# Performance work log

Hardware: AMD Instinct MI355X
Metric: run time of the kernel (lower is better)

## Reference

```python
import jax, jax.numpy as jnp
import numpy as np

N, E, DIN, DH, DOUT, NB = 50000, 400000, 32, 128, 16, 2

def setup_inputs() -> dict:
    key = jax.random.key(0)
    ks = jax.random.split(key, 16)
    s = 0.05
    inp = {
        "inputs": jax.random.normal(ks[0], (N, DIN), jnp.float32),
        "frames": jax.random.normal(ks[1], (N, 3, 3), jnp.float32),
        "edge_index": jax.random.randint(ks[2], (2, E), 0, N, jnp.int32),
        # GraphNet in/out projections
        "win": jax.random.normal(ks[3], (DIN, DH), jnp.float32) * s,
        "bin_": jnp.zeros((DH,), jnp.float32),
        "wout": jax.random.normal(ks[4], (DH, DOUT), jnp.float32) * s,
        "bout": jnp.zeros((DOUT,), jnp.float32),
        # per-block EdgeConv params, stacked over NB blocks
        # mlp1: Linear(2*DH, DH) -> ReLU -> Linear(DH, DH) -> ReLU -> Linear(DH, DH)
        "w1a": jax.random.normal(ks[5], (NB, 2 * DH, DH), jnp.float32) * s,
        "b1a": jnp.zeros((NB, DH), jnp.float32),
        "w1b": jax.random.normal(ks[6], (NB, DH, DH), jnp.float32) * s,
        "b1b": jnp.zeros((NB, DH), jnp.float32),
        "w1c": jax.random.normal(ks[7], (NB, DH, DH), jnp.float32) * s,
        "b1c": jnp.zeros((NB, DH), jnp.float32),
        # mlp2: Linear(DH, DH) -> ReLU -> Linear(DH, DH)
        "w2a": jax.random.normal(ks[8], (NB, DH, DH), jnp.float32) * s,
        "b2a": jnp.zeros((NB, DH), jnp.float32),
        "w2b": jax.random.normal(ks[9], (NB, DH, DH), jnp.float32) * s,
        "b2b": jnp.zeros((NB, DH), jnp.float32),
    }
    return inp


def reference(inputs, frames, edge_index, win, bin_, wout, bout,
              w1a, b1a, w1b, b1b, w1c, b1c, w2a, b2a, w2b, b2b):
    src = edge_index[0]  # j: message source
    dst = edge_index[1]  # i: aggregation target (PyG convention)
    x = inputs @ win + bin_  # [N, DH]
    for b in range(NB):
        x_j = x[src]  # [E, DH] gather
        x_i = x[dst]  # [E, DH] gather
        m = jnp.concatenate([x_j, x_i], axis=-1)  # [E, 2*DH]
        m = jax.nn.relu(m @ w1a[b] + b1a[b])
        m = jax.nn.relu(m @ w1b[b] + b1b[b])
        m = m @ w1c[b] + b1c[b]  # [E, DH]
        agg = jax.ops.segment_sum(m, dst, num_segments=N)  # aggr='add'
        h = jax.nn.relu(agg @ w2a[b] + b2a[b])
        x = h @ w2b[b] + b2b[b]
    return x @ wout + bout  # [N, DOUT]
```

## Files before the change

### kernel.cpp

```cpp
#include <hip/hip_runtime.h>

#define NN 50000
#define NE 400000
#define DIN 32
#define DH  128
#define DOUT 16
#define NB  2
#define NBLK 49

typedef _Float16 half8 __attribute__((ext_vector_type(8)));
typedef float    f32x4 __attribute__((ext_vector_type(4)));

#define FENCE() asm volatile("s_waitcnt lgkmcnt(0)" ::: "memory")
#define MFMA16(a, b, c) __builtin_amdgcn_mfma_f32_16x16x32_f16((a), (b), (c), 0, 0, 0)

__global__ void k_node_proj(const float* __restrict__ inp,
                            const float* __restrict__ win,
                            const float* __restrict__ bin,
                            _Float16* __restrict__ x16) {
    int gid = blockIdx.x * blockDim.x + threadIdx.x;
    if (gid >= NN * DH) return;
    int n = gid >> 7, h = gid & 127;
    float acc = bin[h];
    const float* row = inp + (size_t)n * DIN;
#pragma unroll
    for (int k = 0; k < DIN; ++k) acc = fmaf(row[k], win[k * DH + h], acc);
    x16[gid] = (_Float16)acc;
}

__global__ void k_wprep(const float* __restrict__ w1a, const float* __restrict__ w1b,
                        const float* __restrict__ w1c, const float* __restrict__ w2a,
                        const float* __restrict__ w2b, _Float16* __restrict__ wf) {
    int c = blockIdx.x * blockDim.x + threadIdx.x;
    if (c >= NB * 12288) return;
    int b = c / 12288, r = c % 12288;
    int tt = r >> 9, rem = r & 511;
    const float* W; int t;
    if (tt < 8)       { W = w1a + (size_t)b * 2 * DH * DH; t = tt; }
    else if (tt < 12) { W = w1b + (size_t)b * DH * DH; t = tt - 8; }
    else if (tt < 16) { W = w1c + (size_t)b * DH * DH; t = tt - 12; }
    else if (tt < 20) { W = w2a + (size_t)b * DH * DH; t = tt - 16; }
    else              { W = w2b + (size_t)b * DH * DH; t = tt - 20; }
    bool perm = (tt >= 8 && tt < 16);
    int n = rem >> 6, l = rem & 63;
    int col = n * 16 + (l & 15);
    half8 v;
#pragma unroll
    for (int j = 0; j < 8; ++j) {
        int row = perm ? ((2 * t + (j >> 2)) * 16 + (l >> 4) * 4 + (j & 3))
                       : (t * 32 + (l >> 4) * 8 + j);
        v[j] = (_Float16)W[(size_t)row * DH + col];
    }
    *(half8*)(wf + (size_t)c * 8) = v;
}

__global__ void k_woutprep(const float* __restrict__ wout, _Float16* __restrict__ wf) {
    int c = threadIdx.x;
    int t = c >> 6, l = c & 63;
    half8 v;
#pragma unroll
    for (int j = 0; j < 8; ++j)
        v[j] = (_Float16)wout[(size_t)(t * 32 + (l >> 4) * 8 + j) * DOUT + (l & 15)];
    *(half8*)(wf + (size_t)c * 8) = v;
}

__global__ void k_hist(const int* __restrict__ dstI, int* __restrict__ deg) {
    int e = blockIdx.x * blockDim.x + threadIdx.x;
    if (e < NE) atomicAdd(&deg[dstI[e]], 1);
}

__global__ void __launch_bounds__(1024) k_scanA(const int* __restrict__ deg,
                                                int* __restrict__ bsum) {
    __shared__ int ws[16];
    int tid = threadIdx.x, wv = tid >> 6, l = tid & 63;
    int i = blockIdx.x * 1024 + tid;
    int v = (i < NN) ? deg[i] : 0;
#pragma unroll
    for (int off = 32; off; off >>= 1) v += __shfl_down(v, off);
    if (l == 0) ws[wv] = v;
    __syncthreads();
    if (tid == 0) {
        int s = 0;
#pragma unroll
        for (int k = 0; k < 16; ++k) s += ws[k];
        bsum[blockIdx.x] = s;
    }
}

__global__ void k_scanB(const int* __restrict__ bsum, int* __restrict__ boff) {
    int l = threadIdx.x;
    int v = (l < NBLK) ? bsum[l] : 0;
    int s = v;
#pragma unroll
    for (int off = 1; off < 64; off <<= 1) {
        int t = __shfl_up(s, off);
        if (l >= off) s += t;
    }
    if (l < NBLK) boff[l] = s - v;
}

__global__ void __launch_bounds__(1024) k_scanC(const int* __restrict__ deg,
                                                const int* __restrict__ boff,
                                                int* __restrict__ cur) {
    __shared__ int ws[16];
    int tid = threadIdx.x, wv = tid >> 6, l = tid & 63;
    int i = blockIdx.x * 1024 + tid;
    int v = (i < NN) ? deg[i] : 0;
    int s = v;
#pragma unroll
    for (int off = 1; off < 64; off <<= 1) {
        int t = __shfl_up(s, off);
        if (l >= off) s += t;
    }
    if (l == 63) ws[wv] = s;
    __syncthreads();
    if (wv == 0) {
        int t = (l < 16) ? ws[l] : 0;
#pragma unroll
        for (int off = 1; off < 16; off <<= 1) {
            int u = __shfl_up(t, off);
            if (l >= off) t += u;
        }
        if (l < 16) ws[l] = t;
    }
    __syncthreads();
    int base = boff[blockIdx.x] + (wv ? ws[wv - 1] : 0);
    if (i < NN) cur[i] = base + s - v;
}

__global__ void k_scatter(const int* __restrict__ srcI, const int* __restrict__ dstI,
                          int* __restrict__ cur, int* __restrict__ eS,
                          int* __restrict__ eD) {
    int e = blockIdx.x * blockDim.x + threadIdx.x;
    if (e >= NE) return;
    int d = dstI[e];
    int p = atomicAdd(&cur[d], 1);
    eS[p] = srcI[e];
    eD[p] = d;
}

__global__ void __launch_bounds__(256, 4) k_edge8(
    const _Float16* __restrict__ xin,
    const int* __restrict__ eS, const int* __restrict__ eD,
    const half8* __restrict__ wfa, const half8* __restrict__ wfb,
    const half8* __restrict__ wfc,
    const float* __restrict__ b1a, const float* __restrict__ b1b,
    const float* __restrict__ b1c,
    float* __restrict__ agg) {
    __shared__ _Float16 sm[8192];
    __shared__ int slotT[4][64];

    const int tid = threadIdx.x, wv = tid >> 6, l = tid & 63;
    const int lm = l & 15, lk = l >> 4;
    const int nb = wv * 2;
    const int ebase = blockIdx.x * 64;

    int srcs[4], dsts[4];
#pragma unroll
    for (int s = 0; s < 4; ++s) {
        srcs[s] = eS[ebase + s * 16 + lm];
        dsts[s] = eD[ebase + s * 16 + lm];
    }

    int dl = eD[ebase + l];
    int prev = __shfl(dl, (l == 0) ? 0 : l - 1);
    bool bit = ((l & 31) == 0) ? true : (dl != prev);
    unsigned long long bal = __ballot(bit);
    unsigned mlo = (unsigned)bal, mhi = (unsigned)(bal >> 32);
    unsigned myM = (l < 32) ? mlo : mhi;
    int ll = l & 31;
    int slot_l = __popc(myM << (31 - ll)) - 1;
    if (bit) slotT[wv][(l >> 5) * 32 + slot_l] = dl;
    int nlo = __popc(mlo), nhi = __popc(mhi);

    const f32x4 z = {0.f, 0.f, 0.f, 0.f};
    f32x4 acc[4][2];
    half8 aC[4], aN[4], wC[2], wN[2];

#pragma unroll
    for (int s = 0; s < 4; ++s)
#pragma unroll
        for (int q = 0; q < 2; ++q) acc[s][q] = z;
#pragma unroll
    for (int s = 0; s < 4; ++s)
        aC[s] = *(const half8*)(xin + (size_t)srcs[s] * DH + lk * 8);
#pragma unroll
    for (int q = 0; q < 2; ++q) wC[q] = wfa[(size_t)(nb + q) * 64 + l];

    for (int t = 0; t < 8; ++t) {
        if (t < 7) {
            int t1 = t + 1;
#pragma unroll
            for (int s = 0; s < 4; ++s) {
                int node = (t1 < 4) ? srcs[s] : dsts[s];
                aN[s] = *(const half8*)(xin + (size_t)node * DH + (t1 & 3) * 32 + lk * 8);
            }
#pragma unroll
            for (int q = 0; q < 2; ++q)
                wN[q] = wfa[(size_t)(t1 * 8 + nb + q) * 64 + l];
        }
#pragma unroll
        for (int q = 0; q < 2; ++q)
#pragma unroll
            for (int s = 0; s < 4; ++s)
                acc[s][q] = MFMA16(wC[q], aC[s], acc[s][q]);
#pragma unroll
        for (int s = 0; s < 4; ++s) aC[s] = aN[s];
#pragma unroll
        for (int q = 0; q < 2; ++q) wC[q] = wN[q];
    }
    {
        float4 B0 = *(const float4*)(b1a + nb * 16 + lk * 4);
        float4 B1 = *(const float4*)(b1a + (nb + 1) * 16 + lk * 4);
#pragma unroll
        for (int s = 0; s < 4; ++s) {
            half8 v;
#pragma unroll
            for (int j = 0; j < 4; ++j) {
                v[j]     = (_Float16)fmaxf(acc[s][0][j] + (&B0.x)[j], 0.f);
                v[4 + j] = (_Float16)fmaxf(acc[s][1][j] + (&B1.x)[j], 0.f);
            }
            *(half8*)&sm[((wv * 4 + s) * 64 + l) * 8] = v;
        }
    }
    __syncthreads();

#pragma unroll
    for (int s = 0; s < 4; ++s)
#pragma unroll
        for (int q = 0; q < 2; ++q) acc[s][q] = z;
#pragma unroll
    for (int q = 0; q < 2; ++q) wC[q] = wfb[(size_t)(nb + q) * 64 + l];
    for (int t = 0; t < 4; ++t) {
        if (t < 3)
#pragma unroll
            for (int q = 0; q < 2; ++q)
                wN[q] = wfb[(size_t)((t + 1) * 8 + nb + q) * 64 + l];
#pragma unroll
        for (int s = 0; s < 4; ++s)
            aC[s] = *(const half8*)&sm[((t * 4 + s) * 64 + l) * 8];
#pragma unroll
        for (int q = 0; q < 2; ++q)
#pragma unroll
            for (int s = 0; s < 4; ++s)
                acc[s][q] = MFMA16(wC[q], aC[s], acc[s][q]);
#pragma unroll
        for (int q = 0; q < 2; ++q) wC[q] = wN[q];
    }
    __syncthreads();
    {
        float4 B0 = *(const float4*)(b1b + nb * 16 + lk * 4);
        float4 B1 = *(const float4*)(b1b + (nb + 1) * 16 + lk * 4);
#pragma unroll
        for (int s = 0; s < 4; ++s) {
            half8 v;
#pragma unroll
            for (int j = 0; j < 4; ++j) {
                v[j]     = (_Float16)fmaxf(acc[s][0][j] + (&B0.x)[j], 0.f);
                v[4 + j] = (_Float16)fmaxf(acc[s][1][j] + (&B1.x)[j], 0.f);
            }
            *(half8*)&sm[((wv * 4 + s) * 64 + l) * 8] = v;
        }
    }
    __syncthreads();

#pragma unroll
    for (int s = 0; s < 4; ++s)
#pragma unroll
        for (int q = 0; q < 2; ++q) acc[s][q] = z;
#pragma unroll
    for (int q = 0; q < 2; ++q) wC[q] = wfc[(size_t)(nb + q) * 64 + l];
    for (int t = 0; t < 4; ++t) {
        if (t < 3)
#pragma unroll
            for (int q = 0; q < 2; ++q)
                wN[q] = wfc[(size_t)((t + 1) * 8 + nb + q) * 64 + l];
#pragma unroll
        for (int s = 0; s < 4; ++s)
            aC[s] = *(const half8*)&sm[((t * 4 + s) * 64 + l) * 8];
#pragma unroll
        for (int q = 0; q < 2; ++q)
#pragma unroll
            for (int s = 0; s < 4; ++s)
                acc[s][q] = MFMA16(wC[q], aC[s], acc[s][q]);
#pragma unroll
        for (int q = 0; q < 2; ++q) wC[q] = wN[q];
    }
    __syncthreads();

    {
        float4 C0 = *(const float4*)(b1c + nb * 16 + lk * 4);
        float4 C1 = *(const float4*)(b1c + (nb + 1) * 16 + lk * 4);
#pragma unroll
        for (int s = 0; s < 4; ++s) {
            int h = s >> 1;
            int ldb = (s & 1) * 32 + (lm >> 3) * 16;
#pragma unroll
            for (int q = 0; q < 2; ++q) {
#pragma unroll
                for (int j = 0; j < 4; ++j) {
                    int idx = wv * 2048 +
                              ((h * 2 + q) * 64 + ldb + lk * 4 + j) * 8 + (lm & 7);
                    idx ^= (lm >> 3) << 4;
                    float bv = q ? (&C1.x)[j] : (&C0.x)[j];
                    sm[idx] = (_Float16)(acc[s][q][j] + bv);
                }
            }
        }
    }
    FENCE();

#pragma unroll
    for (int h = 0; h < 2; ++h) {
        const int nsl = h ? nhi : nlo;
        half8 ind0, ind1;
#pragma unroll
        for (int e8 = 0; e8 < 8; ++e8) {
            int se = __shfl(slot_l, h * 32 + lk * 8 + e8);
            ind0[e8] = (se == lm)      ? (_Float16)1.f : (_Float16)0.f;
            ind1[e8] = (se == lm + 16) ? (_Float16)1.f : (_Float16)0.f;
        }
        int4 dv  = *(const int4*)&slotT[wv][h * 32 + lk * 4];
        int4 dv2 = *(const int4*)&slotT[wv][h * 32 + 16 + lk * 4];
        int dS[4], dS2[4];
#pragma unroll
        for (int r = 0; r < 4; ++r) {
            int s0 = lk * 4 + r;
            dS[r]  = (s0 < nsl && s0 < 16) ? (&dv.x)[r] : -1;
            dS2[r] = (16 + s0 < nsl) ? (&dv2.x)[r] : -1;
        }
#pragma unroll
        for (int q = 0; q < 2; ++q) {
            int g = nb + q;
            int bidx = (wv * 2048 + ((h * 2 + q) * 64 + l) * 8) ^ (((l >> 4) & 1) << 4);
            half8 bfrag = *(const half8*)&sm[bidx];
            f32x4 p = MFMA16(ind0, bfrag, z);
#pragma unroll
            for (int r = 0; r < 4; ++r)
                if (dS[r] >= 0)
                    unsafeAtomicAdd(agg + (size_t)dS[r] * DH + g * 16 + lm, p[r]);
            if (nsl > 16) {
                f32x4 p2 = MFMA16(ind1, bfrag, z);
#pragma unroll
                for (int r = 0; r < 4; ++r)
                    if (dS2[r] >= 0)
                        unsafeAtomicAdd(agg + (size_t)dS2[r] * DH + g * 16 + lm, p2[r]);
            }
        }
    }
}

template <bool LAST>
__global__ void __launch_bounds__(256, 4) k_node_mfma(
    const float* __restrict__ agg,
    const half8* __restrict__ wfa, const half8* __restrict__ wfb,
    const float* __restrict__ b2a, const float* __restrict__ b2b,
    _Float16* __restrict__ xo,
    const half8* __restrict__ woutf, const float* __restrict__ bout,
    float* __restrict__ out) {
    __shared__ _Float16 sM[4][2048];
    const int tid = threadIdx.x, wv = tid >> 6, l = tid & 63;
    const int lm = l & 15, lk = l >> 4;
    const int n0 = (blockIdx.x * 4 + wv) * 16;
    if (n0 >= NN) return;
    int nodeA = n0 + lm;
    if (nodeA >= NN) nodeA = NN - 1;

    float b2ar[8], b2br[8];
#pragma unroll
    for (int n = 0; n < 8; ++n) {
        b2ar[n] = b2a[n * 16 + lm];
        b2br[n] = b2b[n * 16 + lm];
    }

    const f32x4 z = {0.f, 0.f, 0.f, 0.f};
    f32x4 acc[8];
#pragma unroll
    for (int n = 0; n < 8; ++n) acc[n] = z;

    for (int t = 0; t < 4; ++t) {
        const float* ap = agg + (size_t)nodeA * DH + t * 32 + lk * 8;
        float4 v0 = *(const float4*)ap;
        float4 v1 = *(const float4*)(ap + 4);
        half8 a;
        a[0] = (_Float16)v0.x; a[1] = (_Float16)v0.y;
        a[2] = (_Float16)v0.z; a[3] = (_Float16)v0.w;
        a[4] = (_Float16)v1.x; a[5] = (_Float16)v1.y;
        a[6] = (_Float16)v1.z; a[7] = (_Float16)v1.w;
        const half8* wp = wfa + (size_t)t * 512 + l;
#pragma unroll
        for (int n = 0; n < 8; ++n) acc[n] = MFMA16(a, wp[n * 64], acc[n]);
    }
    _Float16* sm = sM[wv];
#pragma unroll
    for (int n = 0; n < 8; ++n) {
        int base = ((n >> 1) * 64 + ((n & 1) * 2 + (lm >> 3)) * 16 + lk * 4) * 8 +
                   (lm & 7);
#pragma unroll
        for (int j = 0; j < 4; ++j)
            sm[base + j * 8] = (_Float16)fmaxf(acc[n][j] + b2ar[n], 0.f);
    }
    FENCE();
#pragma unroll
    for (int n = 0; n < 8; ++n) acc[n] = z;
    for (int t = 0; t < 4; ++t) {
        half8 a = *(const half8*)&sm[(t * 64 + l) * 8];
        const half8* wp = wfb + (size_t)t * 512 + l;
#pragma unroll
        for (int n = 0; n < 8; ++n) acc[n] = MFMA16(a, wp[n * 64], acc[n]);
    }
    if (!LAST) {
#pragma unroll
        for (int n = 0; n < 8; ++n) {
#pragma unroll
            for (int j = 0; j < 4; ++j) {
                int nd = n0 + lk * 4 + j;
                if (nd < NN)
                    xo[(size_t)nd * DH + n * 16 + lm] = (_Float16)(acc[n][j] + b2br[n]);
            }
        }
    } else {
        FENCE();
#pragma unroll
        for (int n = 0; n < 8; ++n) {
            int base = ((n >> 1) * 64 + ((n & 1) * 2 + (lm >> 3)) * 16 + lk * 4) * 8 +
                       (lm & 7);
#pragma unroll
            for (int j = 0; j < 4; ++j)
                sm[base + j * 8] = (_Float16)(acc[n][j] + b2br[n]);
        }
        FENCE();
        f32x4 ao = z;
        for (int t = 0; t < 4; ++t) {
            half8 a = *(const half8*)&sm[(t * 64 + l) * 8];
            ao = MFMA16(a, woutf[t * 64 + l], ao);
        }
        float bo = bout[lm];
#pragma unroll
        for (int j = 0; j < 4; ++j) {
            int nd = n0 + lk * 4 + j;
            if (nd < NN) out[(size_t)nd * DOUT + lm] = ao[j] + bo;
        }
    }
}

extern "C" void kernel_launch(void* const* d_in, const int* in_sizes, int n_in,
                              void* d_out, int out_size, void* d_ws, size_t ws_size,
                              hipStream_t stream) {
    const float* inputs = (const float*)d_in[0];
    const int* eidx = (const int*)d_in[2];
    const int* srcI = eidx;
    const int* dstI = eidx + NE;
    const float* win  = (const float*)d_in[3];
    const float* bin_ = (const float*)d_in[4];
    const float* wout = (const float*)d_in[5];
    const float* bout = (const float*)d_in[6];
    const float* w1a = (const float*)d_in[7];
    const float* b1a = (const float*)d_in[8];
    const float* w1b = (const float*)d_in[9];
    const float* b1b = (const float*)d_in[10];
    const float* w1c = (const float*)d_in[11];
    const float* b1c = (const float*)d_in[12];
    const float* w2a = (const float*)d_in[13];
    const float* b2a = (const float*)d_in[14];
    const float* w2b = (const float*)d_in[15];
    const float* b2b = (const float*)d_in[16];

    char* p = (char*)d_ws;
    _Float16* xa = (_Float16*)p;    p += (size_t)NN * DH * 2;
    _Float16* xb = (_Float16*)p;    p += (size_t)NN * DH * 2;
    _Float16* wfAll = (_Float16*)p; p += ((size_t)NB * 12288 + 256) * 16;
    float* agg   = (float*)p;       p += (size_t)NN * DH * 4;
    int* deg     = (int*)p;         p += (size_t)NN * 4;
    int* cur     = (int*)p;         p += (size_t)NN * 4;
    int* bsum    = (int*)p;         p += 256;
    int* boff    = (int*)p;         p += 256;
    int* eSrt    = (int*)p;         p += (size_t)NE * 4;
    int* eDrt    = (int*)p;         p += (size_t)NE * 4;
    float* out   = (float*)d_out;
    _Float16* wfW = wfAll + (size_t)NB * 12288 * 8;

    k_wprep<<<(NB * 12288 + 255) / 256, 256, 0, stream>>>(w1a, w1b, w1c, w2a, w2b, wfAll);
    k_woutprep<<<1, 256, 0, stream>>>(wout, wfW);
    k_node_proj<<<(NN * DH + 255) / 256, 256, 0, stream>>>(inputs, win, bin_, xa);

    hipMemsetAsync(deg, 0, (size_t)NN * 4, stream);
    k_hist<<<(NE + 255) / 256, 256, 0, stream>>>(dstI, deg);
    k_scanA<<<NBLK, 1024, 0, stream>>>(deg, bsum);
    k_scanB<<<1, 64, 0, stream>>>(bsum, boff);
    k_scanC<<<NBLK, 1024, 0, stream>>>(deg, boff, cur);
    k_scatter<<<(NE + 255) / 256, 256, 0, stream>>>(srcI, dstI, cur, eSrt, eDrt);

    for (int b = 0; b < NB; ++b) {
        const _Float16* xi = (b & 1) ? xb : xa;
        _Float16*       xo = (b & 1) ? xa : xb;
        hipMemsetAsync(agg, 0, (size_t)NN * DH * 4, stream);
        const half8* whalf = (const half8*)(wfAll + (size_t)b * 12288 * 8);
        k_edge8<<<NE / 64, 256, 0, stream>>>(
            xi, eSrt, eDrt, whalf, whalf + 4096, whalf + 6144,
            b1a + (size_t)b * DH, b1b + (size_t)b * DH, b1c + (size_t)b * DH,
            agg);
        if (b < NB - 1)
            k_node_mfma<false><<<(NN + 63) / 64, 256, 0, stream>>>(
                agg, whalf + 8192, whalf + 10240,
                b2a + (size_t)b * DH, b2b + (size_t)b * DH,
                xo, (const half8*)wfW, bout, out);
        else
            k_node_mfma<true><<<(NN + 63) / 64, 256, 0, stream>>>(
                agg, whalf + 8192, whalf + 10240,
                b2a + (size_t)b * DH, b2b + (size_t)b * DH,
                xo, (const half8*)wfW, bout, out);
    }
}
```

Before: 367.0 us.

## Make edge MLP kernel persistent with weights held in registers

The per-tile edge kernel becomes a persistent kernel with a fixed grid of 512 blocks that grid-strides over 64-edge tiles. Each wave loads its slice of all three MLP weight matrices into registers once and reuses them for every tile, instead of streaming weight fragments from global memory per tile. Edge index loads become one coalesced load per lane followed by shuffles. The added register pressure lowers the launch bound to 2 blocks per CU, which reduces the latency hiding available for the random feature gathers and the atomics.

After: 394.1 us. 1.07x slower.

```diff
diff --git a/kernel.cpp b/kernel.cpp
--- a/kernel.cpp
+++ b/kernel.cpp
@@ -7,6 +7,8 @@
 #define DOUT 16
 #define NB  2
 #define NBLK 49
+#define NTILE (NE / 64)
+#define EGRID 512
 
 typedef _Float16 half8 __attribute__((ext_vector_type(8)));
 typedef float    f32x4 __attribute__((ext_vector_type(4)));
@@ -139,7 +141,7 @@
     eD[p] = d;
 }
 
-__global__ void __launch_bounds__(256, 4) k_edge8(
+__global__ void __launch_bounds__(256, 2) k_edge9(
     const _Float16* __restrict__ xin,
     const int* __restrict__ eS, const int* __restrict__ eD,
     const half8* __restrict__ wfa, const half8* __restrict__ wfb,
@@ -153,198 +155,193 @@
     const int tid = threadIdx.x, wv = tid >> 6, l = tid & 63;
     const int lm = l & 15, lk = l >> 4;
     const int nb = wv * 2;
-    const int ebase = blockIdx.x * 64;
-
-    int srcs[4], dsts[4];
-#pragma unroll
-    for (int s = 0; s < 4; ++s) {
-        srcs[s] = eS[ebase + s * 16 + lm];
-        dsts[s] = eD[ebase + s * 16 + lm];
-    }
-
-    int dl = eD[ebase + l];
-    int prev = __shfl(dl, (l == 0) ? 0 : l - 1);
-    bool bit = ((l & 31) == 0) ? true : (dl != prev);
-    unsigned long long bal = __ballot(bit);
-    unsigned mlo = (unsigned)bal, mhi = (unsigned)(bal >> 32);
-    unsigned myM = (l < 32) ? mlo : mhi;
-    int ll = l & 31;
-    int slot_l = __popc(myM << (31 - ll)) - 1;
-    if (bit) slotT[wv][(l >> 5) * 32 + slot_l] = dl;
-    int nlo = __popc(mlo), nhi = __popc(mhi);
+
+    half8 W1[16], W2[8], W3[8];
+#pragma unroll
+    for (int i = 0; i < 16; ++i)
+        W1[i] = wfa[(size_t)((i >> 1) * 8 + nb + (i & 1)) * 64 + l];
+#pragma unroll
+    for (int i = 0; i < 8; ++i)
+        W2[i] = wfb[(size_t)((i >> 1) * 8 + nb + (i & 1)) * 64 + l];
+#pragma unroll
+    for (int i = 0; i < 8; ++i)
+        W3[i] = wfc[(size_t)((i >> 1) * 8 + nb + (i & 1)) * 64 + l];
 
     const f32x4 z = {0.f, 0.f, 0.f, 0.f};
-    f32x4 acc[4][2];
-    half8 aC[4], aN[4], wC[2], wN[2];
-
-#pragma unroll
-    for (int s = 0; s < 4; ++s)
-#pragma unroll
-        for (int q = 0; q < 2; ++q) acc[s][q] = z;
-#pragma unroll
-    for (int s = 0; s < 4; ++s)
-        aC[s] = *(const half8*)(xin + (size_t)srcs[s] * DH + lk * 8);
-#pragma unroll
-    for (int q = 0; q < 2; ++q) wC[q] = wfa[(size_t)(nb + q) * 64 + l];
-
-    for (int t = 0; t < 8; ++t) {
-        if (t < 7) {
-            int t1 = t + 1;
+
+    for (int tile = blockIdx.x; tile < NTILE; tile += EGRID) {
+        const int ebase = tile * 64;
+
+        const int sl_ = eS[ebase + l];
+        const int dl  = eD[ebase + l];
+        int srcs[4], dsts[4];
+#pragma unroll
+        for (int s = 0; s < 4; ++s) {
+            srcs[s] = __shfl(sl_, s * 16 + lm);
+            dsts[s] = __shfl(dl,  s * 16 + lm);
+        }
+
+        int prev = __shfl(dl, (l == 0) ? 0 : l - 1);
+        bool bit = ((l & 31) == 0) ? true : (dl != prev);
+        unsigned long long bal = __ballot(bit);
+        unsigned mlo = (unsigned)bal, mhi = (unsigned)(bal >> 32);
+        unsigned myM = (l < 32) ? mlo : mhi;
+        int ll = l & 31;
+        int slot_l = __popc(myM << (31 - ll)) - 1;
+        if (bit) slotT[wv][(l >> 5) * 32 + slot_l] = dl;
+        int nlo = __popc(mlo), nhi = __popc(mhi);
+
+        f32x4 acc[4][2];
+        half8 aC[4], aN[4];
+
+#pragma unroll
+        for (int s = 0; s < 4; ++s)
+#pragma unroll
+            for (int q = 0; q < 2; ++q) acc[s][q] = z;
+#pragma unroll
+        for (int s = 0; s < 4; ++s)
+            aC[s] = *(const half8*)(xin + (size_t)srcs[s] * DH + lk * 8);
+#pragma unroll
+        for (int t = 0; t < 8; ++t) {
+            if (t < 7) {
+                int t1 = t + 1;
+#pragma unroll
+                for (int s = 0; s < 4; ++s) {
+                    int node = (t1 < 4) ? srcs[s] : dsts[s];
+                    aN[s] = *(const half8*)(xin + (size_t)node * DH + (t1 & 3) * 32 + lk * 8);
+                }
+            }
+#pragma unroll
+            for (int q = 0; q < 2; ++q)
+#pragma unroll
+                for (int s = 0; s < 4; ++s)
+                    acc[s][q] = MFMA16(W1[t * 2 + q], aC[s], acc[s][q]);
+#pragma unroll
+            for (int s = 0; s < 4; ++s) aC[s] = aN[s];
+        }
+        {
+            float4 B0 = *(const float4*)(b1a + nb * 16 + lk * 4);
+            float4 B1 = *(const float4*)(b1a + (nb + 1) * 16 + lk * 4);
 #pragma unroll
             for (int s = 0; s < 4; ++s) {
-                int node = (t1 < 4) ? srcs[s] : dsts[s];
-                aN[s] = *(const half8*)(xin + (size_t)node * DH + (t1 & 3) * 32 + lk * 8);
-            }
+                half8 v;
+#pragma unroll
+                for (int j = 0; j < 4; ++j) {
+                    v[j]     = (_Float16)fmaxf(acc[s][0][j] + (&B0.x)[j], 0.f);
+                    v[4 + j] = (_Float16)fmaxf(acc[s][1][j] + (&B1.x)[j], 0.f);
+                }
+                *(half8*)&sm[((wv * 4 + s) * 64 + l) * 8] = v;
+            }
+        }
+        __syncthreads();
+
+#pragma unroll
+        for (int s = 0; s < 4; ++s)
+#pragma unroll
+            for (int q = 0; q < 2; ++q) acc[s][q] = z;
+#pragma unroll
+        for (int t = 0; t < 4; ++t) {
+#pragma unroll
+            for (int s = 0; s < 4; ++s)
+                aC[s] = *(const half8*)&sm[((t * 4 + s) * 64 + l) * 8];
 #pragma unroll
             for (int q = 0; q < 2; ++q)
-                wN[q] = wfa[(size_t)(t1 * 8 + nb + q) * 64 + l];
-        }
-#pragma unroll
-        for (int q = 0; q < 2; ++q)
+#pragma unroll
+                for (int s = 0; s < 4; ++s)
+                    acc[s][q] = MFMA16(W2[t * 2 + q], aC[s], acc[s][q]);
+        }
+        __syncthreads();
+        {
+            float4 B0 = *(const float4*)(b1b + nb * 16 + lk * 4);
+            float4 B1 = *(const float4*)(b1b + (nb + 1) * 16 + lk * 4);
+#pragma unroll
+            for (int s = 0; s < 4; ++s) {
+                half8 v;
+#pragma unroll
+                for (int j = 0; j < 4; ++j) {
+                    v[j]     = (_Float16)fmaxf(acc[s][0][j] + (&B0.x)[j], 0.f);
+                    v[4 + j] = (_Float16)fmaxf(acc[s][1][j] + (&B1.x)[j], 0.f);
+                }
+                *(half8*)&sm[((wv * 4 + s) * 64 + l) * 8] = v;
+            }
+        }
+        __syncthreads();
+
+#pragma unroll
+        for (int s = 0; s < 4; ++s)
+#pragma unroll
+            for (int q = 0; q < 2; ++q) acc[s][q] = z;
+#pragma unroll
+        for (int t = 0; t < 4; ++t) {
 #pragma unroll
             for (int s = 0; s < 4; ++s)
-                acc[s][q] = MFMA16(wC[q], aC[s], acc[s][q]);
-#pragma unroll
-        for (int s = 0; s < 4; ++s) aC[s] = aN[s];
-#pragma unroll
-        for (int q = 0; q < 2; ++q) wC[q] = wN[q];
-    }
-    {
-        float4 B0 = *(const float4*)(b1a + nb * 16 + lk * 4);
-        float4 B1 = *(const float4*)(b1a + (nb + 1) * 16 + lk * 4);
-#pragma unroll
-        for (int s = 0; s < 4; ++s) {
-            half8 v;
-#pragma unroll
-            for (int j = 0; j < 4; ++j) {
-                v[j]     = (_Float16)fmaxf(acc[s][0][j] + (&B0.x)[j], 0.f);
-                v[4 + j] = (_Float16)fmaxf(acc[s][1][j] + (&B1.x)[j], 0.f);
-            }
-            *(half8*)&sm[((wv * 4 + s) * 64 + l) * 8] = v;
-        }
-    }
-    __syncthreads();
-
-#pragma unroll
-    for (int s = 0; s < 4; ++s)
-#pragma unroll
-        for (int q = 0; q < 2; ++q) acc[s][q] = z;
-#pragma unroll
-    for (int q = 0; q < 2; ++q) wC[q] = wfb[(size_t)(nb + q) * 64 + l];
-    for (int t = 0; t < 4; ++t) {
-        if (t < 3)
+                aC[s] = *(const half8*)&sm[((t * 4 + s) * 64 + l) * 8];
 #pragma unroll
             for (int q = 0; q < 2; ++q)
-                wN[q] = wfb[(size_t)((t + 1) * 8 + nb + q) * 64 + l];
-#pragma unroll
-        for (int s = 0; s < 4; ++s)
-            aC[s] = *(const half8*)&sm[((t * 4 + s) * 64 + l) * 8];
-#pragma unroll
-        for (int q = 0; q < 2; ++q)
-#pragma unroll
-            for (int s = 0; s < 4; ++s)
-                acc[s][q] = MFMA16(wC[q], aC[s], acc[s][q]);
-#pragma unroll
-        for (int q = 0; q < 2; ++q) wC[q] = wN[q];
-    }
-    __syncthreads();
-    {
-        float4 B0 = *(const float4*)(b1b + nb * 16 + lk * 4);
-        float4 B1 = *(const float4*)(b1b + (nb + 1) * 16 + lk * 4);
-#pragma unroll
-        for (int s = 0; s < 4; ++s) {
-            half8 v;
-#pragma unroll
-            for (int j = 0; j < 4; ++j) {
-                v[j]     = (_Float16)fmaxf(acc[s][0][j] + (&B0.x)[j], 0.f);
-                v[4 + j] = (_Float16)fmaxf(acc[s][1][j] + (&B1.x)[j], 0.f);
-            }
-            *(half8*)&sm[((wv * 4 + s) * 64 + l) * 8] = v;
-        }
-    }
-    __syncthreads();
-
-#pragma unroll
-    for (int s = 0; s < 4; ++s)
-#pragma unroll
-        for (int q = 0; q < 2; ++q) acc[s][q] = z;
-#pragma unroll
-    for (int q = 0; q < 2; ++q) wC[q] = wfc[(size_t)(nb + q) * 64 + l];
-    for (int t = 0; t < 4; ++t) {
-        if (t < 3)
-#pragma unroll
-            for (int q = 0; q < 2; ++q)
-                wN[q] = wfc[(size_t)((t + 1) * 8 + nb + q) * 64 + l];
-#pragma unroll
-        for (int s = 0; s < 4; ++s)
-            aC[s] = *(const half8*)&sm[((t * 4 + s) * 64 + l) * 8];
-#pragma unroll
-        for (int q = 0; q < 2; ++q)
-#pragma unroll
-            for (int s = 0; s < 4; ++s)
-                acc[s][q] = MFMA16(wC[q], aC[s], acc[s][q]);
-#pragma unroll
-        for (int q = 0; q < 2; ++q) wC[q] = wN[q];
-    }
-    __syncthreads();
-
-    {
-        float4 C0 = *(const float4*)(b1c + nb * 16 + lk * 4);
-        float4 C1 = *(const float4*)(b1c + (nb + 1) * 16 + lk * 4);
-#pragma unroll
-        for (int s = 0; s < 4; ++s) {
-            int h = s >> 1;
-            int ldb = (s & 1) * 32 + (lm >> 3) * 16;
+#pragma unroll
+                for (int s = 0; s < 4; ++s)
+                    acc[s][q] = MFMA16(W3[t * 2 + q], aC[s], acc[s][q]);
+        }
+        __syncthreads();
+
+        {
+            float4 C0 = *(const float4*)(b1c + nb * 16 + lk * 4);
+            float4 C1 = *(const float4*)(b1c + (nb + 1) * 16 + lk * 4);
+#pragma unroll
+            for (int s = 0; s < 4; ++s) {
+                int h = s >> 1;
+                int ldb = (s & 1) * 32 + (lm >> 3) * 16;
+#pragma unroll
+                for (int q = 0; q < 2; ++q) {
+#pragma unroll
+                    for (int j = 0; j < 4; ++j) {
+                        int idx = wv * 2048 +
+                                  ((h * 2 + q) * 64 + ldb + lk * 4 + j) * 8 + (lm & 7);
+                        idx ^= (lm >> 3) << 4;
+                        float bv = q ? (&C1.x)[j] : (&C0.x)[j];
+                        sm[idx] = (_Float16)(acc[s][q][j] + bv);
+                    }
+                }
+            }
+        }
+        FENCE();
+
+#pragma unroll
+        for (int h = 0; h < 2; ++h) {
+            const int nsl = h ? nhi : nlo;
+            half8 ind0, ind1;
+#pragma unroll
+            for (int e8 = 0; e8 < 8; ++e8) {
+                int se = __shfl(slot_l, h * 32 + lk * 8 + e8);
+                ind0[e8] = (se == lm)      ? (_Float16)1.f : (_Float16)0.f;
+                ind1[e8] = (se == lm + 16) ? (_Float16)1.f : (_Float16)0.f;
+            }
+            int4 dv  = *(const int4*)&slotT[wv][h * 32 + lk * 4];
+            int4 dv2 = *(const int4*)&slotT[wv][h * 32 + 16 + lk * 4];
+            int dS[4], dS2[4];
+#pragma unroll
+            for (int r = 0; r < 4; ++r) {
+                int s0 = lk * 4 + r;
+                dS[r]  = (s0 < nsl && s0 < 16) ? (&dv.x)[r] : -1;
+                dS2[r] = (16 + s0 < nsl) ? (&dv2.x)[r] : -1;
+            }
 #pragma unroll
             for (int q = 0; q < 2; ++q) {
-#pragma unroll
-                for (int j = 0; j < 4; ++j) {
-                    int idx = wv * 2048 +
-                              ((h * 2 + q) * 64 + ldb + lk * 4 + j) * 8 + (lm & 7);
-                    idx ^= (lm >> 3) << 4;
-                    float bv = q ? (&C1.x)[j] : (&C0.x)[j];
-                    sm[idx] = (_Float16)(acc[s][q][j] + bv);
+                int g = nb + q;
+                int bidx = (wv * 2048 + ((h * 2 + q) * 64 + l) * 8) ^ (((l >> 4) & 1) << 4);
+                half8 bfrag = *(const half8*)&sm[bidx];
+                f32x4 p = MFMA16(ind0, bfrag, z);
+#pragma unroll
+                for (int r = 0; r < 4; ++r)
+                    if (dS[r] >= 0)
+                        unsafeAtomicAdd(agg + (size_t)dS[r] * DH + g * 16 + lm, p[r]);
+                if (nsl > 16) {
+                    f32x4 p2 = MFMA16(ind1, bfrag, z);
+#pragma unroll
+                    for (int r = 0; r < 4; ++r)
+                        if (dS2[r] >= 0)
+                            unsafeAtomicAdd(agg + (size_t)dS2[r] * DH + g * 16 + lm, p2[r]);
                 }
-            }
-        }
-    }
-    FENCE();
-
-#pragma unroll
-    for (int h = 0; h < 2; ++h) {
-        const int nsl = h ? nhi : nlo;
-        half8 ind0, ind1;
-#pragma unroll
-        for (int e8 = 0; e8 < 8; ++e8) {
-            int se = __shfl(slot_l, h * 32 + lk * 8 + e8);
-            ind0[e8] = (se == lm)      ? (_Float16)1.f : (_Float16)0.f;
-            ind1[e8] = (se == lm + 16) ? (_Float16)1.f : (_Float16)0.f;
-        }
-        int4 dv  = *(const int4*)&slotT[wv][h * 32 + lk * 4];
-        int4 dv2 = *(const int4*)&slotT[wv][h * 32 + 16 + lk * 4];
-        int dS[4], dS2[4];
-#pragma unroll
-        for (int r = 0; r < 4; ++r) {
-            int s0 = lk * 4 + r;
-            dS[r]  = (s0 < nsl && s0 < 16) ? (&dv.x)[r] : -1;
-            dS2[r] = (16 + s0 < nsl) ? (&dv2.x)[r] : -1;
-        }
-#pragma unroll
-        for (int q = 0; q < 2; ++q) {
-            int g = nb + q;
-            int bidx = (wv * 2048 + ((h * 2 + q) * 64 + l) * 8) ^ (((l >> 4) & 1) << 4);
-            half8 bfrag = *(const half8*)&sm[bidx];
-            f32x4 p = MFMA16(ind0, bfrag, z);
-#pragma unroll
-            for (int r = 0; r < 4; ++r)
-                if (dS[r] >= 0)
-                    unsafeAtomicAdd(agg + (size_t)dS[r] * DH + g * 16 + lm, p[r]);
-            if (nsl > 16) {
-                f32x4 p2 = MFMA16(ind1, bfrag, z);
-#pragma unroll
-                for (int r = 0; r < 4; ++r)
-                    if (dS2[r] >= 0)
-                        unsafeAtomicAdd(agg + (size_t)dS2[r] * DH + g * 16 + lm, p2[r]);
             }
         }
     }
@@ -496,7 +493,7 @@
         _Float16*       xo = (b & 1) ? xa : xb;
         hipMemsetAsync(agg, 0, (size_t)NN * DH * 4, stream);
         const half8* whalf = (const half8*)(wfAll + (size_t)b * 12288 * 8);
-        k_edge8<<<NE / 64, 256, 0, stream>>>(
+        k_edge9<<<EGRID, 256, 0, stream>>>(
             xi, eSrt, eDrt, whalf, whalf + 4096, whalf + 6144,
             b1a + (size_t)b * DH, b1b + (size_t)b * DH, b1c + (size_t)b * DH,
             agg);
```
